# Kernel optimization log

Hardware: AMD Instinct MI355X
Metric: run time of the kernel (lower is better)

Reference implementation:

```python
import math
import jax, jax.numpy as jnp
import numpy as np

SR = 22050
FRAME_SIZE = 1025  # n_fft=2048 -> 1025 bins
MAX_FILTER_SIZE = 20
B, T = 32, 2000


def _to_mel(freq):
    return 2595.0 * np.log10(1.0 + freq / 700.0)


def build_transform_matrix(frame_size=FRAME_SIZE, sr=SR, max_filter_size=MAX_FILTER_SIZE):
    # Banded Gaussian smoothing matrix; filter width grows in mel scale (<= max_filter_size).
    freq = np.linspace(0.0, sr / 2.0, num=frame_size, endpoint=True)
    mel = _to_mel(freq)
    raw = (mel - mel[0]) / (mel[-1] - mel[0]) * (max_filter_size - 1) + 1
    mtx = np.zeros((frame_size, frame_size), dtype=np.float64)
    for i in range(frame_size):
        fs = int(math.floor(raw[i])) // 2 * 2 + 1  # odd filter size
        if fs == 1:
            mtx[i, i] = 1.0
            continue
        sigma = (fs - 1) / 6.0
        # replicate scipy.ndimage.gaussian_filter1d (order=0, mode='reflect', truncate=4)
        radius = int(4.0 * sigma + 0.5)
        x = np.arange(-radius, radius + 1)
        k = np.exp(-0.5 * (x / sigma) ** 2)
        k /= k.sum()
        imp = np.zeros(fs)
        imp[fs // 2] = 1.0
        # scipy 'reflect' == numpy 'symmetric'; symmetric kernel so convolve == correlate
        f = np.convolve(np.pad(imp, radius, mode='symmetric'), k, mode='valid')
        start, end = max(0, i - fs // 2), min(i + fs // 2 + 1, frame_size)
        f_start = start - i + fs // 2
        f_end = end - i + fs // 2
        f = f[f_start:f_end]
        mtx[i, start:end] = f / f.sum()
    return mtx.astype(np.float32)


def setup_inputs() -> dict:
    key = jax.random.key(0)
    k1, k2 = jax.random.split(key)
    model_output = jax.random.normal(k1, (B, FRAME_SIZE, T), dtype=jnp.float32)
    target = jax.random.normal(k2, (B, FRAME_SIZE, T), dtype=jnp.float32)
    transform_matrix = jnp.asarray(build_transform_matrix())
    return {"model_output": model_output, "target": target,
            "transform_matrix": transform_matrix}


def reference(model_output, target, transform_matrix):
    # db_to_amp(x) = 10**(x/20); (db_to_amp(x))**2 = 10**(x/10)
    mo = jnp.power(jnp.float32(10.0), model_output / jnp.float32(10.0))
    tg = jnp.power(jnp.float32(10.0), target / jnp.float32(10.0))
    diff = mo - tg  # [B, F, T]
    transformed = jnp.einsum('fk,bkt->bft', transform_matrix, diff)
    return jnp.mean(transformed ** 2)
```

## Files before the change

### kernel.cpp

```cpp
#include <hip/hip_runtime.h>
#include <math.h>


#define B_N 32
#define F_N 1025
#define T_N 2000

#define NOUT   106
#define NCHUNK 10
#define NT     256
#define CT     512
#define CST    24

#define LOG2_10_DIV10 0.33219280948873623f

__global__ __launch_bounds__(NT, 4)
void mel_mse_stream(const float* __restrict__ mo_g, const float* __restrict__ tg_g,
                    const float* __restrict__ M, float* __restrict__ partials) {
    __shared__ float sm[NOUT * CST];
    __shared__ float red[NT];

    const int tid = threadIdx.x;
    const int t0  = blockIdx.x * CT;
    const int f0  = blockIdx.y * NOUT;
    const int b   = blockIdx.z;
    const int t   = t0 + tid * 2;
    const bool active = (t + 1 < T_N);

    for (int i = tid; i < NOUT * CST; i += NT) {
        const int row = i / CST;
        const int j   = i - row * CST;
        const int f   = f0 + row;
        const int k   = f - 10 + j;
        float v = 0.0f;
        if (j < 21 && f < F_N && k >= 0 && k < F_N) v = M[(size_t)f * F_N + k];
        sm[i] = v;
    }
    __syncthreads();

    const int    tc      = active ? t : 0;
    const size_t colbase = ((size_t)b * F_N) * (size_t)T_N + tc;
    const int    base    = f0 - 10;

    float2 w[21];
    float  acc = 0.f;

    auto LOAD = [&](int r) -> float2 {
        int g = base + r;
        const float mask = (active && g >= 0 && g < F_N) ? 1.f : 0.f;
        g = g < 0 ? 0 : (g >= F_N ? F_N - 1 : g);
        const size_t off = colbase + (size_t)g * T_N;
        const float2 a = *reinterpret_cast<const float2*>(mo_g + off);
        const float2 c = *reinterpret_cast<const float2*>(tg_g + off);
        float2 d;
        d.x = (exp2f(a.x * LOG2_10_DIV10) - exp2f(c.x * LOG2_10_DIV10)) * mask;
        d.y = (exp2f(a.y * LOG2_10_DIV10) - exp2f(c.y * LOG2_10_DIV10)) * mask;
        return d;
    };
    auto OUT = [&](int r_out, int s0) {
        if (f0 + r_out < F_N) {
            float cf[24];
            const float4* c4 = reinterpret_cast<const float4*>(&sm[r_out * CST]);
#pragma unroll
            for (int q = 0; q < 6; ++q)
                *reinterpret_cast<float4*>(&cf[4 * q]) = c4[q];
            float2 o = make_float2(0.f, 0.f);
#pragma unroll
            for (int j = 0; j < 21; ++j) {
                const float2 wv = w[(s0 + j) % 21];
                o.x = fmaf(cf[j], wv.x, o.x);
                o.y = fmaf(cf[j], wv.y, o.y);
            }
            acc = fmaf(o.x, o.x, fmaf(o.y, o.y, acc));
        }
    };

#pragma unroll
    for (int i = 0; i < 21; ++i) w[i] = LOAD(i);
    OUT(0, 0);

    for (int m = 1; m < 6; ++m) {
        const int rb = m * 21;
#pragma unroll
        for (int i = 0; i < 21; ++i) {
            w[i] = LOAD(rb + i);
            OUT(rb + i - 20, (i + 1) % 21);
        }
    }

    red[tid] = acc;
    __syncthreads();
    for (int s = NT / 2; s > 0; s >>= 1) {
        if (tid < s) red[tid] += red[tid + s];
        __syncthreads();
    }
    if (tid == 0) {
        const int bid = blockIdx.x + gridDim.x * (blockIdx.y + gridDim.y * blockIdx.z);
        partials[bid] = red[0];
    }
}

__global__ void mel_mse_reduce(const float* __restrict__ partials, int n,
                               float* __restrict__ out) {
    __shared__ double red[256];
    double s = 0.0;
    for (int i = threadIdx.x; i < n; i += 256) s += (double)partials[i];
    red[threadIdx.x] = s;
    __syncthreads();
    for (int st = 128; st > 0; st >>= 1) {
        if (threadIdx.x < st) red[threadIdx.x] += red[threadIdx.x + st];
        __syncthreads();
    }
    if (threadIdx.x == 0)
        out[0] = (float)(red[0] / (double)((long long)B_N * F_N * T_N));
}

extern "C" void kernel_launch(void* const* d_in, const int* in_sizes, int n_in,
                              void* d_out, int out_size, void* d_ws, size_t ws_size,
                              hipStream_t stream) {
    const float* mo = (const float*)d_in[0];
    const float* tg = (const float*)d_in[1];
    const float* M  = (const float*)d_in[2];
    float* out      = (float*)d_out;
    float* partials = (float*)d_ws;

    dim3 grid((T_N + CT - 1) / CT,
              NCHUNK,
              B_N);
    const int nparts = grid.x * grid.y * grid.z;

    mel_mse_stream<<<grid, NT, 0, stream>>>(mo, tg, M, partials);
    mel_mse_reduce<<<1, 256, 0, stream>>>(partials, nparts, out);
}
```

Before: 132.0 us.

## Prefetch input rows in registers and read precomputed band coefficients from global memory

Adds a small pre-kernel that extracts the 21-wide band of the transform matrix into a compact global buffer. The streaming kernel then reads coefficients from that buffer instead of staging them in shared memory behind a barrier. Global loads of model_output and target are issued three rows ahead of the exp2 and subtract step, so memory latency can overlap with compute. Out-of-range rows are no longer masked per element, because their band coefficients are already zero; invalid columns are masked once at the final accumulation. The cost is one extra kernel launch and more registers held for the prefetch slots, which could reduce occupancy.

```diff
diff --git a/kernel.cpp b/kernel.cpp
--- a/kernel.cpp
+++ b/kernel.cpp
@@ -7,17 +7,30 @@
 #define T_N 2000
 
 #define NOUT   106
+#define ROWS   126
 #define NCHUNK 10
 #define NT     256
 #define CT     512
-#define CST    24
+#define PF     3
+#define CBS    24
+#define BANDROWS (NCHUNK * NOUT)
 
-#define LOG2_10_DIV10 0.33219280948873623f
+#define K_E 0.33219280948873623f
+
+__global__ void build_band(const float* __restrict__ M, float* __restrict__ band) {
+    const int idx = blockIdx.x * 256 + threadIdx.x;
+    if (idx >= BANDROWS * CBS) return;
+    const int f = idx / CBS;
+    const int j = idx - f * CBS;
+    const int k = f - 10 + j;
+    float v = 0.f;
+    if (j < 21 && f < F_N && k >= 0 && k < F_N) v = M[(size_t)f * F_N + k];
+    band[idx] = v;
+}
 
 __global__ __launch_bounds__(NT, 4)
 void mel_mse_stream(const float* __restrict__ mo_g, const float* __restrict__ tg_g,
-                    const float* __restrict__ M, float* __restrict__ partials) {
-    __shared__ float sm[NOUT * CST];
+                    const float* __restrict__ band, float* __restrict__ partials) {
     __shared__ float red[NT];
 
     const int tid = threadIdx.x;
@@ -25,70 +38,64 @@
     const int f0  = blockIdx.y * NOUT;
     const int b   = blockIdx.z;
     const int t   = t0 + tid * 2;
-    const bool active = (t + 1 < T_N);
+    const bool colv = (t + 1 < T_N);
+    const int  tc   = colv ? t : 0;
+    const int  base = f0 - 10;
 
-    for (int i = tid; i < NOUT * CST; i += NT) {
-        const int row = i / CST;
-        const int j   = i - row * CST;
-        const int f   = f0 + row;
-        const int k   = f - 10 + j;
-        float v = 0.0f;
-        if (j < 21 && f < F_N && k >= 0 && k < F_N) v = M[(size_t)f * F_N + k];
-        sm[i] = v;
-    }
-    __syncthreads();
-
-    const int    tc      = active ? t : 0;
     const size_t colbase = ((size_t)b * F_N) * (size_t)T_N + tc;
-    const int    base    = f0 - 10;
 
     float2 w[21];
+    float2 ra[PF], rc[PF];
     float  acc = 0.f;
 
-    auto LOAD = [&](int r) -> float2 {
-        int g = base + r;
-        const float mask = (active && g >= 0 && g < F_N) ? 1.f : 0.f;
-        g = g < 0 ? 0 : (g >= F_N ? F_N - 1 : g);
+    auto ISSUE = [&](int n, int s) {
+        int g = base + n;
+        g = g < 0 ? 0 : (g > F_N - 1 ? F_N - 1 : g);
         const size_t off = colbase + (size_t)g * T_N;
-        const float2 a = *reinterpret_cast<const float2*>(mo_g + off);
-        const float2 c = *reinterpret_cast<const float2*>(tg_g + off);
-        float2 d;
-        d.x = (exp2f(a.x * LOG2_10_DIV10) - exp2f(c.x * LOG2_10_DIV10)) * mask;
-        d.y = (exp2f(a.y * LOG2_10_DIV10) - exp2f(c.y * LOG2_10_DIV10)) * mask;
-        return d;
+        ra[s] = *reinterpret_cast<const float2*>(mo_g + off);
+        rc[s] = *reinterpret_cast<const float2*>(tg_g + off);
     };
-    auto OUT = [&](int r_out, int s0) {
-        if (f0 + r_out < F_N) {
-            float cf[24];
-            const float4* c4 = reinterpret_cast<const float4*>(&sm[r_out * CST]);
+    auto CONS = [&](int s, int ws) {
+        const float2 a = ra[s], c = rc[s];
+        w[ws].x = exp2f(a.x * K_E) - exp2f(c.x * K_E);
+        w[ws].y = exp2f(a.y * K_E) - exp2f(c.y * K_E);
+    };
+    auto OUT = [&](int frow, int s0) {
+        const float4* c4 = reinterpret_cast<const float4*>(band + (size_t)frow * CBS);
+        float cf[24];
 #pragma unroll
-            for (int q = 0; q < 6; ++q)
-                *reinterpret_cast<float4*>(&cf[4 * q]) = c4[q];
-            float2 o = make_float2(0.f, 0.f);
+        for (int q = 0; q < 6; ++q)
+            *reinterpret_cast<float4*>(&cf[4 * q]) = c4[q];
+        float2 o = make_float2(0.f, 0.f);
 #pragma unroll
-            for (int j = 0; j < 21; ++j) {
-                const float2 wv = w[(s0 + j) % 21];
-                o.x = fmaf(cf[j], wv.x, o.x);
-                o.y = fmaf(cf[j], wv.y, o.y);
-            }
-            acc = fmaf(o.x, o.x, fmaf(o.y, o.y, acc));
+        for (int j = 0; j < 21; ++j) {
+            const float2 wv = w[(s0 + j) % 21];
+            o.x = fmaf(cf[j], wv.x, o.x);
+            o.y = fmaf(cf[j], wv.y, o.y);
         }
+        acc = fmaf(o.x, o.x, fmaf(o.y, o.y, acc));
     };
 
 #pragma unroll
-    for (int i = 0; i < 21; ++i) w[i] = LOAD(i);
-    OUT(0, 0);
+    for (int i = 0; i < PF; ++i) ISSUE(i, i);
 
+#pragma unroll
+    for (int i = 0; i < 21; ++i) {
+        CONS(i % PF, i);
+        ISSUE(i + PF, i % PF);
+        if (i == 20) OUT(f0, 0);
+    }
     for (int m = 1; m < 6; ++m) {
-        const int rb = m * 21;
+        const int nb = m * 21;
 #pragma unroll
         for (int i = 0; i < 21; ++i) {
-            w[i] = LOAD(rb + i);
-            OUT(rb + i - 20, (i + 1) % 21);
+            CONS(i % PF, i);
+            ISSUE(nb + i + PF, i % PF);
+            OUT(f0 + nb + i - 20, (i + 1) % 21);
         }
     }
 
-    red[tid] = acc;
+    red[tid] = colv ? acc : 0.f;
     __syncthreads();
     for (int s = NT / 2; s > 0; s >>= 1) {
         if (tid < s) red[tid] += red[tid + s];
@@ -122,13 +129,17 @@
     const float* tg = (const float*)d_in[1];
     const float* M  = (const float*)d_in[2];
     float* out      = (float*)d_out;
-    float* partials = (float*)d_ws;
+
+    float* band     = (float*)d_ws;
+    float* partials = (float*)((char*)d_ws + 102400);
+
+    build_band<<<(BANDROWS * CBS + 255) / 256, 256, 0, stream>>>(M, band);
 
     dim3 grid((T_N + CT - 1) / CT,
               NCHUNK,
               B_N);
     const int nparts = grid.x * grid.y * grid.z;
 
-    mel_mse_stream<<<grid, NT, 0, stream>>>(mo, tg, M, partials);
+    mel_mse_stream<<<grid, NT, 0, stream>>>(mo, tg, band, partials);
     mel_mse_reduce<<<1, 256, 0, stream>>>(partials, nparts, out);
 }
```

Result: faster. 124.6 us (-5.6%).
